# Optimization experiments

Hardware: AMD Instinct MI355X
Metric: run time of the kernel (lower is better)

## Reference

```python
import jax, jax.numpy as jnp
import numpy as np

DIM = 1024
DEPTH = 6
HEADS = 16
MLP = 4096
HEAD_DIM = DIM // HEADS
SCALE = HEAD_DIM ** -0.5
EPS = 1e-5


def _ln(x, g, b):
    m = jnp.mean(x, axis=-1, keepdims=True)
    v = jnp.mean(jnp.square(x - m), axis=-1, keepdims=True)
    return (x - m) * jax.lax.rsqrt(v + EPS) * g + b


def setup_inputs() -> dict:
    key = jax.random.key(0)
    ks = jax.random.split(key, 16)
    B, N = 4, 1024
    s_d = 1.0 / np.sqrt(DIM)
    s_m = 1.0 / np.sqrt(MLP)
    inp = {
        "x1": jax.random.normal(ks[0], (B, N, DIM), jnp.float32),
        "x2": jax.random.normal(ks[1], (B, N, DIM), jnp.float32),
        # stacked per-layer params; Linear weights stored as [in, out]
        "ln1_g": jnp.ones((DEPTH, DIM), jnp.float32),
        "ln1_b": jnp.zeros((DEPTH, DIM), jnp.float32),
        "wq": jax.random.normal(ks[2], (DEPTH, DIM, DIM), jnp.float32) * s_d,
        "wk": jax.random.normal(ks[3], (DEPTH, DIM, DIM), jnp.float32) * s_d,
        "wv": jax.random.normal(ks[4], (DEPTH, DIM, DIM), jnp.float32) * s_d,
        "wo": jax.random.normal(ks[5], (DEPTH, DIM, DIM), jnp.float32) * s_d,
        "bo": jnp.zeros((DEPTH, DIM), jnp.float32),
        "ln2_g": jnp.ones((DEPTH, DIM), jnp.float32),
        "ln2_b": jnp.zeros((DEPTH, DIM), jnp.float32),
        "w1": jax.random.normal(ks[6], (DEPTH, DIM, MLP), jnp.float32) * s_d,
        "b1": jnp.zeros((DEPTH, MLP), jnp.float32),
        "w2": jax.random.normal(ks[7], (DEPTH, MLP, DIM), jnp.float32) * s_m,
        "b2": jnp.zeros((DEPTH, DIM), jnp.float32),
    }
    return inp


def _split_heads(t):
    b, n, _ = t.shape
    return t.reshape(b, n, HEADS, HEAD_DIM).transpose(0, 2, 1, 3)  # b h n d


def reference(x1, x2, ln1_g, ln1_b, wq, wk, wv, wo, bo, ln2_g, ln2_b, w1, b1, w2, b2):
    # dropout disabled (eval mode)
    for i in range(DEPTH):
        # PreNorm(MCA): same LayerNorm params applied to x1 and x2
        n1 = _ln(x1, ln1_g[i], ln1_b[i])
        n2 = _ln(x2, ln1_g[i], ln1_b[i])
        q = _split_heads(n1 @ wq[i])
        k = _split_heads(n2 @ wk[i])
        v = _split_heads(n2 @ wv[i])
        dots = jnp.einsum('bhqd,bhkd->bhqk', q, k) * SCALE
        attn = jax.nn.softmax(dots, axis=-1)
        out = jnp.einsum('bhqk,bhkd->bhqd', attn, v)
        b, h, n, d = out.shape
        out = out.transpose(0, 2, 1, 3).reshape(b, n, h * d)
        x1 = out @ wo[i] + bo[i] + x1
        # PreNorm(FeedForward)
        nf = _ln(x1, ln2_g[i], ln2_b[i])
        hdn = jax.nn.gelu(nf @ w1[i] + b1[i], approximate=False)
        x1 = hdn @ w2[i] + b2[i] + x1
    return x1
```

## Files before the change

### kernel.cpp

```cpp
#include <hip/hip_runtime.h>
#include <stdint.h>

#define N_SEQ 1024
#define N_TOK 4096
#define ATT_SCALE 0.125f

typedef unsigned short u16;
typedef __attribute__((ext_vector_type(8))) short short8;
typedef __attribute__((ext_vector_type(4))) short short4v;
typedef __attribute__((ext_vector_type(4))) float f32x4;

__device__ __forceinline__ u16 f2bf(float f) {
  uint32_t u = __float_as_uint(f);
  u += 0x7fffu + ((u >> 16) & 1u);
  return (u16)(u >> 16);
}

__device__ __forceinline__ void gload16(const void* g, void* lds) {
  __builtin_amdgcn_global_load_lds(
      (const __attribute__((address_space(1))) unsigned int*)g,
      (__attribute__((address_space(3))) unsigned int*)lds, 16, 0, 0);
}

__global__ void copy_f32_kernel(const float* __restrict__ in, float* __restrict__ out) {
  int i = blockIdx.x * 256 + threadIdx.x;
  ((float4*)out)[i] = ((const float4*)in)[i];
}

__global__ __launch_bounds__(256) void tconv_kernel(const float* __restrict__ src,
                                                    u16* __restrict__ dst,
                                                    int K, int NN, size_t dstLS) {
  __shared__ u16 tile[64][68];
  int n0 = blockIdx.x * 64, k0 = blockIdx.y * 64, L = blockIdx.z;
  const float* s = src + (size_t)L * K * NN;
  u16* d = dst + (size_t)L * dstLS;
  int t = threadIdx.x;
  int rr = t >> 4, cc = (t & 15) * 4;
#pragma unroll
  for (int ii = 0; ii < 4; ii++) {
    int kl = rr + ii * 16;
    float4 v = *(const float4*)&s[(size_t)(k0 + kl) * NN + n0 + cc];
    tile[cc + 0][kl] = f2bf(v.x);
    tile[cc + 1][kl] = f2bf(v.y);
    tile[cc + 2][kl] = f2bf(v.z);
    tile[cc + 3][kl] = f2bf(v.w);
  }
  __syncthreads();
#pragma unroll
  for (int ii = 0; ii < 4; ii++) {
    int nl = rr + ii * 16;
    short4v o;
    o.x = (short)tile[nl][cc + 0];
    o.y = (short)tile[nl][cc + 1];
    o.z = (short)tile[nl][cc + 2];
    o.w = (short)tile[nl][cc + 3];
    *(short4v*)&d[(size_t)(n0 + nl) * K + k0 + cc] = o;
  }
}

__global__ __launch_bounds__(256) void ln_kernel(const float* __restrict__ x,
                                                 const float* __restrict__ g,
                                                 const float* __restrict__ b,
                                                 u16* __restrict__ out) {
  int row = blockIdx.x;
  const float* xr = x + (size_t)row * 1024;
  int t = threadIdx.x;
  float4 v = *(const float4*)&xr[t * 4];
  float s = v.x + v.y + v.z + v.w;
  float sq = v.x * v.x + v.y * v.y + v.z * v.z + v.w * v.w;
#pragma unroll
  for (int m = 1; m < 64; m <<= 1) {
    s += __shfl_xor(s, m, 64);
    sq += __shfl_xor(sq, m, 64);
  }
  __shared__ float ps[8];
  int w = t >> 6;
  if ((t & 63) == 0) { ps[w] = s; ps[4 + w] = sq; }
  __syncthreads();
  s = ps[0] + ps[1] + ps[2] + ps[3];
  sq = ps[4] + ps[5] + ps[6] + ps[7];
  float mean = s * (1.0f / 1024.0f);
  float var = sq * (1.0f / 1024.0f) - mean * mean;
  float rs = rsqrtf(var + 1e-5f);
  float4 gv = *(const float4*)&g[t * 4];
  float4 bv = *(const float4*)&b[t * 4];
  short4v o;
  o.x = (short)f2bf((v.x - mean) * rs * gv.x + bv.x);
  o.y = (short)f2bf((v.y - mean) * rs * gv.y + bv.y);
  o.z = (short)f2bf((v.z - mean) * rs * gv.z + bv.z);
  o.w = (short)f2bf((v.w - mean) * rs * gv.w + bv.w);
  *(short4v*)&out[(size_t)row * 1024 + t * 4] = o;
}

template <int MODE>
__global__ __launch_bounds__(256, 3) void gemmM(const u16* __restrict__ A,
                                                const u16* __restrict__ Bt,
                                                u16* __restrict__ outb,
                                                float* __restrict__ outf,
                                                const float* __restrict__ bias,
                                                const float* __restrict__ resid,
                                                int N, int K) {
  constexpr int AT = 128 * 32;
  __shared__ u16 smem[2 * 2 * AT];

  int t = threadIdx.x, lane = t & 63, w = t >> 6;
  int wm = w >> 1, wn = w & 1;
  const u16* Ag = A + (size_t)(blockIdx.y * 128) * K;
  const u16* Bg = Bt + (size_t)(blockIdx.x * 128) * K;
  f32x4 acc[4][4] = {};

  auto stage = [&](int d, int k0) {
    u16* ab = smem + d * 2 * AT;
    u16* bb = ab + AT;
#pragma unroll
    for (int l = 0; l < 2; l++) {
      int c = l * 256 + t;
      gload16(Ag + (size_t)(c >> 2) * K + k0 + (c & 3) * 8, ab + c * 8);
    }
#pragma unroll
    for (int l = 0; l < 2; l++) {
      int c = l * 256 + t;
      gload16(Bg + (size_t)(c >> 2) * K + k0 + (c & 3) * 8, bb + c * 8);
    }
  };

  const int NT = K / 32;
  stage(0, 0);
  __syncthreads();

  int buf = 0;
  for (int tt = 0; tt < NT; tt++) {
    if (tt + 1 < NT) stage(buf ^ 1, (tt + 1) * 32);
    const u16* ab = smem + buf * 2 * AT;
    const u16* bb = ab + AT;
    short8 af[4], bf[4];
#pragma unroll
    for (int mi = 0; mi < 4; mi++)
      af[mi] = *(const short8*)&ab[(wm * 64 + mi * 16 + (lane & 15)) * 32 + (lane >> 4) * 8];
#pragma unroll
    for (int ni = 0; ni < 4; ni++)
      bf[ni] = *(const short8*)&bb[(wn * 64 + ni * 16 + (lane & 15)) * 32 + (lane >> 4) * 8];
#pragma unroll
    for (int mi = 0; mi < 4; mi++)
#pragma unroll
      for (int ni = 0; ni < 4; ni++)
        acc[mi][ni] = __builtin_amdgcn_mfma_f32_16x16x32_bf16(af[mi], bf[ni], acc[mi][ni], 0, 0, 0);
    __syncthreads();
    buf ^= 1;
  }

  int r0 = blockIdx.y * 128 + wm * 64 + ((lane >> 4) << 2);
  int c0 = blockIdx.x * 128 + wn * 64 + (lane & 15);
#pragma unroll
  for (int mi = 0; mi < 4; mi++) {
#pragma unroll
    for (int r = 0; r < 4; r++) {
      size_t row = (size_t)(r0 + mi * 16 + r);
#pragma unroll
      for (int ni = 0; ni < 4; ni++) {
        size_t col = (size_t)(c0 + ni * 16);
        size_t idx = row * N + col;
        float val = acc[mi][ni][r];
        if (MODE == 0) {
          outb[idx] = f2bf(val);
        } else if (MODE == 1) {
          outf[idx] = val + bias[col] + resid[idx];
        } else {
          float xg = val + bias[col];
          outb[idx] = f2bf(0.5f * xg * (1.0f + erff(xg * 0.70710678f)));
        }
      }
    }
  }
}

template <int BM, int BN, int WM, int WN, int MODE>
__global__ __launch_bounds__(WM * WN * 64, 2) void gemm8(const u16* __restrict__ A,
                                                         const u16* __restrict__ Bt,
                                                         u16* __restrict__ outb,
                                                         float* __restrict__ outf,
                                                         const float* __restrict__ bias,
                                                         const float* __restrict__ resid,
                                                         int N, int K) {
  constexpr int BK = 64;
  constexpr int NW = WM * WN;
  constexpr int T = NW * 64;
  constexpr int WTM = BM / WM, WTN = BN / WN;
  constexpr int FM = WTM / 16, FN = WTN / 16, HM = FM / 2;
  constexpr int AT = BM * BK, BTL = BN * BK;
  constexpr int LA = AT / 8 / T, LB = BTL / 8 / T;
  constexpr int LTOT = LA + LB;
  __shared__ u16 smem[2 * (AT + BTL)];

  int t = threadIdx.x, lane = t & 63, w = t >> 6;
  int wm = w / WN, wn = w % WN;
  const u16* Ag = A + (size_t)(blockIdx.y * BM) * K;
  const u16* Bg = Bt + (size_t)(blockIdx.x * BN) * K;
  f32x4 acc[FM][FN] = {};

  auto stage = [&](int d, int k0) {
    u16* ab = smem + d * (AT + BTL);
    u16* bb = ab + AT;
#pragma unroll
    for (int l = 0; l < LA; l++) {
      int c = (l * NW + w) * 64 + lane;
      int r = c >> 3, s = c & 7;
      gload16(Ag + (size_t)r * K + k0 + ((s ^ (r & 7)) << 3), ab + (l * NW + w) * 512);
    }
#pragma unroll
    for (int l = 0; l < LB; l++) {
      int c = (l * NW + w) * 64 + lane;
      int r = c >> 3, s = c & 7;
      gload16(Bg + (size_t)r * K + k0 + ((s ^ (r & 7)) << 3), bb + (l * NW + w) * 512);
    }
  };

  auto rdA = [&](const u16* ab, int mi, int ks) {
    int rr = wm * WTM + mi * 16 + (lane & 15);
    int j = ks * 4 + (lane >> 4);
    return *(const short8*)&ab[rr * BK + ((j ^ (rr & 7)) << 3)];
  };
  auto rdB = [&](const u16* bb, int ni, int ks) {
    int rr = wn * WTN + ni * 16 + (lane & 15);
    int j = ks * 4 + (lane >> 4);
    return *(const short8*)&bb[rr * BK + ((j ^ (rr & 7)) << 3)];
  };

  const int NT = K / BK;
  stage(0, 0);
  stage(1, BK);
  __builtin_amdgcn_sched_barrier(0);

  int buf = 0;
  for (int tt = 0; tt < NT; tt++) {
    asm volatile("s_waitcnt vmcnt(%0)" ::"n"(LTOT) : "memory");
    __builtin_amdgcn_s_barrier();
    __builtin_amdgcn_sched_barrier(0);
    const u16* ab = smem + buf * (AT + BTL);
    const u16* bb = ab + AT;
    short8 b0[FN], a0lo[HM], a0hi[HM], b1[FN], a1lo[HM], a1hi[HM];
#pragma unroll
    for (int n = 0; n < FN; n++) b0[n] = rdB(bb, n, 0);
#pragma unroll
    for (int m = 0; m < HM; m++) a0lo[m] = rdA(ab, m, 0);
#pragma unroll
    for (int m = 0; m < HM; m++) a0hi[m] = rdA(ab, HM + m, 0);
    asm volatile("s_waitcnt lgkmcnt(%0)" ::"n"(HM) : "memory");
    __builtin_amdgcn_sched_barrier(0);
#pragma unroll
    for (int n = 0; n < FN; n++) b1[n] = rdB(bb, n, 1);
#pragma unroll
    for (int m = 0; m < HM; m++) a1lo[m] = rdA(ab, m, 1);
    __builtin_amdgcn_s_setprio(1);
#pragma unroll
    for (int m = 0; m < HM; m++)
#pragma unroll
      for (int n = 0; n < FN; n++)
        acc[m][n] = __builtin_amdgcn_mfma_f32_16x16x32_bf16(a0lo[m], b0[n], acc[m][n], 0, 0, 0);
    __builtin_amdgcn_s_setprio(0);
    asm volatile("s_waitcnt lgkmcnt(%0)" ::"n"(FN + HM) : "memory");
    __builtin_amdgcn_sched_barrier(0);
#pragma unroll
    for (int m = 0; m < HM; m++) a1hi[m] = rdA(ab, HM + m, 1);
    __builtin_amdgcn_s_setprio(1);
#pragma unroll
    for (int m = 0; m < HM; m++)
#pragma unroll
      for (int n = 0; n < FN; n++)
        acc[HM + m][n] = __builtin_amdgcn_mfma_f32_16x16x32_bf16(a0hi[m], b0[n], acc[HM + m][n], 0, 0, 0);
    __builtin_amdgcn_s_setprio(0);
    asm volatile("s_waitcnt lgkmcnt(%0)" ::"n"(HM) : "memory");
    __builtin_amdgcn_sched_barrier(0);
    __builtin_amdgcn_s_setprio(1);
#pragma unroll
    for (int m = 0; m < HM; m++)
#pragma unroll
      for (int n = 0; n < FN; n++)
        acc[m][n] = __builtin_amdgcn_mfma_f32_16x16x32_bf16(a1lo[m], b1[n], acc[m][n], 0, 0, 0);
    __builtin_amdgcn_s_setprio(0);
    asm volatile("s_waitcnt lgkmcnt(0)" ::: "memory");
    __builtin_amdgcn_sched_barrier(0);
    __builtin_amdgcn_s_barrier();
    __builtin_amdgcn_sched_barrier(0);
    stage(buf, ((tt + 2) % NT) * BK);
    __builtin_amdgcn_sched_barrier(0);
    __builtin_amdgcn_s_setprio(1);
#pragma unroll
    for (int m = 0; m < HM; m++)
#pragma unroll
      for (int n = 0; n < FN; n++)
        acc[HM + m][n] = __builtin_amdgcn_mfma_f32_16x16x32_bf16(a1hi[m], b1[n], acc[HM + m][n], 0, 0, 0);
    __builtin_amdgcn_s_setprio(0);
    buf ^= 1;
  }

  int r0 = blockIdx.y * BM + wm * WTM + ((lane >> 4) << 2);
  int c0 = blockIdx.x * BN + wn * WTN + (lane & 15);
#pragma unroll
  for (int mi = 0; mi < FM; mi++) {
#pragma unroll
    for (int r = 0; r < 4; r++) {
      size_t row = (size_t)(r0 + mi * 16 + r);
#pragma unroll
      for (int ni = 0; ni < FN; ni++) {
        size_t col = (size_t)(c0 + ni * 16);
        size_t idx = row * N + col;
        float val = acc[mi][ni][r];
        if (MODE == 0) {
          outb[idx] = f2bf(val);
        } else if (MODE == 1) {
          outf[idx] = val + bias[col] + resid[idx];
        } else {
          float xg = val + bias[col];
          outb[idx] = f2bf(0.5f * xg * (1.0f + erff(xg * 0.70710678f)));
        }
      }
    }
  }
}

__global__ __launch_bounds__(256, 4) void attn_kernel(const u16* __restrict__ qb,
                                                      const u16* __restrict__ kvb,
                                                      u16* __restrict__ ob) {
  int qt = blockIdx.x, bh = blockIdx.y;
  int b = bh >> 4, h = bh & 15;
  int t = threadIdx.x, lane = t & 63, w = t >> 6;
  __shared__ u16 Qs[64 * 64];
  __shared__ u16 Ks[64 * 64];
  __shared__ u16 Vt[64 * 64];
  __shared__ u16 Ps[4][16 * 64];

  const u16* qbase = qb + (size_t)b * N_SEQ * 1024 + h * 64;
  const u16* kbase = kvb + (size_t)b * N_SEQ * 2048 + h * 64;
  const u16* vbase = kbase + 1024;
  u16* obase = ob + (size_t)b * N_SEQ * 1024 + h * 64;

  int r = t >> 2, c = (t & 3) * 16;
  {
    const u16* src = qbase + (size_t)(qt * 64 + r) * 1024 + c;
    *(short8*)&Qs[r * 64 + c] = *(const short8*)src;
    *(short8*)&Qs[r * 64 + c + 8] = *(const short8*)(src + 8);
  }
  short8 kreg0, kreg1, vreg0, vreg1;
  {
    const u16* ksrc = kbase + (size_t)r * 2048 + c;
    kreg0 = *(const short8*)ksrc;
    kreg1 = *(const short8*)(ksrc + 8);
    const u16* vsrc = vbase + (size_t)r * 2048 + c;
    vreg0 = *(const short8*)vsrc;
    vreg1 = *(const short8*)(vsrc + 8);
  }
  __syncthreads();
  short8 qa0 = *(const short8*)&Qs[(w * 16 + (lane & 15)) * 64 + (lane >> 4) * 8];
  short8 qa1 = *(const short8*)&Qs[(w * 16 + (lane & 15)) * 64 + 32 + (lane >> 4) * 8];

  f32x4 o[4] = {};
  float m_r[4] = {-1e30f, -1e30f, -1e30f, -1e30f};
  float l_r[4] = {0.0f, 0.0f, 0.0f, 0.0f};

  for (int kt = 0; kt < 16; kt++) {
    if (kt > 0) __syncthreads();
    {
      int jj0 = c >> 3;
      *(short8*)&Ks[r * 64 + ((jj0 ^ (r & 7)) << 3)] = kreg0;
      *(short8*)&Ks[r * 64 + (((jj0 + 1) ^ (r & 7)) << 3)] = kreg1;
#pragma unroll
      for (int j = 0; j < 8; j++) {
        int row = c + j, rowb = c + 8 + j;
        Vt[row * 64 + (((r >> 3) ^ (row & 7)) << 3) + (r & 7)] = (u16)vreg0[j];
        Vt[rowb * 64 + (((r >> 3) ^ (rowb & 7)) << 3) + (r & 7)] = (u16)vreg1[j];
      }
    }
    __syncthreads();
    if (kt < 15) {
      const u16* ksrc = kbase + (size_t)((kt + 1) * 64 + r) * 2048 + c;
      kreg0 = *(const short8*)ksrc;
      kreg1 = *(const short8*)(ksrc + 8);
      const u16* vsrc = vbase + (size_t)((kt + 1) * 64 + r) * 2048 + c;
      vreg0 = *(const short8*)vsrc;
      vreg1 = *(const short8*)(vsrc + 8);
    }

    f32x4 s[4] = {};
#pragma unroll
    for (int kb = 0; kb < 4; kb++) {
      int key = kb * 16 + (lane & 15);
      int jj = lane >> 4;
      short8 k0 = *(const short8*)&Ks[key * 64 + ((jj ^ (key & 7)) << 3)];
      short8 k1 = *(const short8*)&Ks[key * 64 + (((4 + jj) ^ (key & 7)) << 3)];
      s[kb] = __builtin_amdgcn_mfma_f32_16x16x32_bf16(qa0, k0, s[kb], 0, 0, 0);
      s[kb] = __builtin_amdgcn_mfma_f32_16x16x32_bf16(qa1, k1, s[kb], 0, 0, 0);
    }
    float fac[4], rowsum[4];
#pragma unroll
    for (int rr = 0; rr < 4; rr++) {
      float a = fmaxf(fmaxf(s[0][rr], s[1][rr]), fmaxf(s[2][rr], s[3][rr])) * ATT_SCALE;
      a = fmaxf(a, __shfl_xor(a, 1, 64));
      a = fmaxf(a, __shfl_xor(a, 2, 64));
      a = fmaxf(a, __shfl_xor(a, 4, 64));
      a = fmaxf(a, __shfl_xor(a, 8, 64));
      float mn = fmaxf(m_r[rr], a);
      fac[rr] = __expf(m_r[rr] - mn);
      m_r[rr] = mn;
      rowsum[rr] = 0.0f;
    }
#pragma unroll
    for (int kb = 0; kb < 4; kb++) {
      int chunk = 2 * kb + ((lane & 15) >> 3);
#pragma unroll
      for (int rr = 0; rr < 4; rr++) {
        float p = __expf(s[kb][rr] * ATT_SCALE - m_r[rr]);
        rowsum[rr] += p;
        int row = (lane >> 4) * 4 + rr;
        Ps[w][row * 64 + ((chunk ^ (row & 7)) << 3) + (lane & 7)] = f2bf(p);
      }
    }
#pragma unroll
    for (int rr = 0; rr < 4; rr++) {
      float rs = rowsum[rr];
      rs += __shfl_xor(rs, 1, 64);
      rs += __shfl_xor(rs, 2, 64);
      rs += __shfl_xor(rs, 4, 64);
      rs += __shfl_xor(rs, 8, 64);
      l_r[rr] = l_r[rr] * fac[rr] + rs;
      o[0][rr] *= fac[rr];
      o[1][rr] *= fac[rr];
      o[2][rr] *= fac[rr];
      o[3][rr] *= fac[rr];
    }
#pragma unroll
    for (int ks = 0; ks < 2; ks++) {
      int rowp = lane & 15;
      int jj = 4 * ks + (lane >> 4);
      short8 pf = *(const short8*)&Ps[w][rowp * 64 + ((jj ^ (rowp & 7)) << 3)];
#pragma unroll
      for (int db = 0; db < 4; db++) {
        int row = db * 16 + (lane & 15);
        short8 vf = *(const short8*)&Vt[row * 64 + ((jj ^ (row & 7)) << 3)];
        o[db] = __builtin_amdgcn_mfma_f32_16x16x32_bf16(pf, vf, o[db], 0, 0, 0);
      }
    }
  }
#pragma unroll
  for (int rr = 0; rr < 4; rr++) {
    float inv = 1.0f / l_r[rr];
    size_t row = (size_t)(qt * 64 + w * 16 + (lane >> 4) * 4 + rr);
#pragma unroll
    for (int db = 0; db < 4; db++)
      obase[row * 1024 + db * 16 + (lane & 15)] = f2bf(o[db][rr] * inv);
  }
}

extern "C" void kernel_launch(void* const* d_in, const int* in_sizes, int n_in,
                              void* d_out, int out_size, void* d_ws, size_t ws_size,
                              hipStream_t stream) {
  const float* x1 = (const float*)d_in[0];
  const float* x2 = (const float*)d_in[1];
  const float* ln1_g = (const float*)d_in[2];
  const float* ln1_b = (const float*)d_in[3];
  const float* wq = (const float*)d_in[4];
  const float* wk = (const float*)d_in[5];
  const float* wv = (const float*)d_in[6];
  const float* wo = (const float*)d_in[7];
  const float* bo = (const float*)d_in[8];
  const float* ln2_g = (const float*)d_in[9];
  const float* ln2_b = (const float*)d_in[10];
  const float* w1 = (const float*)d_in[11];
  const float* b1 = (const float*)d_in[12];
  const float* w2 = (const float*)d_in[13];
  const float* b2 = (const float*)d_in[14];
  float* xout = (float*)d_out;

  u16* p = (u16*)d_ws;
  u16* wqt = p;  p += (size_t)6 * 1024 * 1024;
  u16* kvt = p;  p += (size_t)6 * 2048 * 1024;
  u16* wot = p;  p += (size_t)6 * 1024 * 1024;
  u16* w1t = p;  p += (size_t)6 * 4096 * 1024;
  u16* w2t = p;  p += (size_t)6 * 1024 * 4096;
  u16* n1 = p;   p += (size_t)N_TOK * 1024;
  u16* n2 = p;   p += (size_t)N_TOK * 1024;
  u16* qbuf = p; p += (size_t)N_TOK * 1024;
  u16* kvbuf = p; p += (size_t)N_TOK * 2048;
  u16* ao = p;   p += (size_t)N_TOK * 1024;
  u16* hid = p;  p += (size_t)N_TOK * 4096;

  dim3 blk(256);
  tconv_kernel<<<dim3(16, 16, 6), blk, 0, stream>>>(wq, wqt, 1024, 1024, (size_t)1024 * 1024);
  tconv_kernel<<<dim3(16, 16, 6), blk, 0, stream>>>(wk, kvt, 1024, 1024, (size_t)2048 * 1024);
  tconv_kernel<<<dim3(16, 16, 6), blk, 0, stream>>>(wv, kvt + (size_t)1024 * 1024, 1024, 1024, (size_t)2048 * 1024);
  tconv_kernel<<<dim3(16, 16, 6), blk, 0, stream>>>(wo, wot, 1024, 1024, (size_t)1024 * 1024);
  tconv_kernel<<<dim3(64, 16, 6), blk, 0, stream>>>(w1, w1t, 1024, 4096, (size_t)4096 * 1024);
  tconv_kernel<<<dim3(16, 64, 6), blk, 0, stream>>>(w2, w2t, 4096, 1024, (size_t)1024 * 4096);
  copy_f32_kernel<<<4096, blk, 0, stream>>>(x1, xout);

  for (int i = 0; i < 6; i++) {
    ln_kernel<<<N_TOK, blk, 0, stream>>>(xout, ln1_g + i * 1024, ln1_b + i * 1024, n1);
    ln_kernel<<<N_TOK, blk, 0, stream>>>(x2, ln1_g + i * 1024, ln1_b + i * 1024, n2);
    gemm8<128, 64, 2, 2, 0><<<dim3(16, 32), blk, 0, stream>>>(
        n1, wqt + (size_t)i * 1024 * 1024, qbuf, nullptr, nullptr, nullptr, 1024, 1024);
    gemm8<128, 128, 2, 2, 0><<<dim3(16, 32), blk, 0, stream>>>(
        n2, kvt + (size_t)i * 2048 * 1024, kvbuf, nullptr, nullptr, nullptr, 2048, 1024);
    attn_kernel<<<dim3(16, 64), blk, 0, stream>>>(qbuf, kvbuf, ao);
    gemm8<128, 64, 2, 2, 1><<<dim3(16, 32), blk, 0, stream>>>(
        ao, wot + (size_t)i * 1024 * 1024, nullptr, xout, bo + i * 1024, xout, 1024, 1024);
    ln_kernel<<<N_TOK, blk, 0, stream>>>(xout, ln2_g + i * 1024, ln2_b + i * 1024, n1);
    gemmM<2><<<dim3(32, 32), blk, 0, stream>>>(
        n1, w1t + (size_t)i * 4096 * 1024, hid, nullptr, b1 + i * 4096, nullptr, 4096, 1024);
    gemm8<128, 64, 2, 2, 1><<<dim3(16, 32), blk, 0, stream>>>(
        hid, w2t + (size_t)i * 1024 * 4096, nullptr, xout, b2 + i * 1024, xout, 1024, 4096);
  }
}
```

Before: 1.575 ms.

## Hoist K/V projections out of layer loop into one batched GEMM, swizzled BK=64 GEMM

K and V depend only on x2 and per-layer weights, so all six LayerNorms of x2 and all six K/V projections are computed up front. The projections run as one z-batched launch with 6144 blocks, replacing six smaller per-layer launches. A new templated GEMM with BK=64, XOR-swizzled LDS layout and 64x128 tiles replaces the old FFN1 GEMM and is also used for the batched K/V GEMM. This needs workspace for six copies of the normalized x2 and six K/V buffers, and it writes and rereads a larger working set through memory.

```diff
diff --git a/kernel.cpp b/kernel.cpp
--- a/kernel.cpp
+++ b/kernel.cpp
@@ -92,74 +92,99 @@
   *(short4v*)&out[(size_t)row * 1024 + t * 4] = o;
 }
 
-template <int MODE>
-__global__ __launch_bounds__(256, 3) void gemmM(const u16* __restrict__ A,
-                                                const u16* __restrict__ Bt,
-                                                u16* __restrict__ outb,
-                                                float* __restrict__ outf,
-                                                const float* __restrict__ bias,
-                                                const float* __restrict__ resid,
-                                                int N, int K) {
-  constexpr int AT = 128 * 32;
-  __shared__ u16 smem[2 * 2 * AT];
+template <int BM, int BN, int WM, int WN, int MAXB, int MODE>
+__global__ __launch_bounds__(WM * WN * 64, MAXB) void gemmS(const u16* __restrict__ A,
+                                                            const u16* __restrict__ Bt,
+                                                            u16* __restrict__ outb,
+                                                            float* __restrict__ outf,
+                                                            const float* __restrict__ bias,
+                                                            const float* __restrict__ resid,
+                                                            int N, int K,
+                                                            size_t zA, size_t zB, size_t zC) {
+  constexpr int BK = 64;
+  constexpr int NW = WM * WN;
+  constexpr int T = NW * 64;
+  constexpr int WTM = BM / WM, WTN = BN / WN;
+  constexpr int FM = WTM / 16, FN = WTN / 16;
+  constexpr int AT = BM * BK, BTL = BN * BK;
+  constexpr int LA = AT / 8 / T, LB = BTL / 8 / T;
+  __shared__ u16 smem[2 * (AT + BTL)];
 
   int t = threadIdx.x, lane = t & 63, w = t >> 6;
-  int wm = w >> 1, wn = w & 1;
-  const u16* Ag = A + (size_t)(blockIdx.y * 128) * K;
-  const u16* Bg = Bt + (size_t)(blockIdx.x * 128) * K;
-  f32x4 acc[4][4] = {};
+  int wm = w / WN, wn = w % WN;
+  size_t z = blockIdx.z;
+  const u16* Ag = A + z * zA + (size_t)(blockIdx.y * BM) * K;
+  const u16* Bg = Bt + z * zB + (size_t)(blockIdx.x * BN) * K;
+  f32x4 acc[FM][FN] = {};
 
   auto stage = [&](int d, int k0) {
-    u16* ab = smem + d * 2 * AT;
+    u16* ab = smem + d * (AT + BTL);
     u16* bb = ab + AT;
 #pragma unroll
-    for (int l = 0; l < 2; l++) {
-      int c = l * 256 + t;
-      gload16(Ag + (size_t)(c >> 2) * K + k0 + (c & 3) * 8, ab + c * 8);
-    }
-#pragma unroll
-    for (int l = 0; l < 2; l++) {
-      int c = l * 256 + t;
-      gload16(Bg + (size_t)(c >> 2) * K + k0 + (c & 3) * 8, bb + c * 8);
+    for (int l = 0; l < LA; l++) {
+      int c = (l * NW + w) * 64 + lane;
+      int r = c >> 3, s = c & 7;
+      gload16(Ag + (size_t)r * K + k0 + ((s ^ (r & 7)) << 3), ab + (l * NW + w) * 512);
+    }
+#pragma unroll
+    for (int l = 0; l < LB; l++) {
+      int c = (l * NW + w) * 64 + lane;
+      int r = c >> 3, s = c & 7;
+      gload16(Bg + (size_t)r * K + k0 + ((s ^ (r & 7)) << 3), bb + (l * NW + w) * 512);
     }
   };
 
-  const int NT = K / 32;
+  auto rdA = [&](const u16* ab, int mi, int ks) {
+    int rr = wm * WTM + mi * 16 + (lane & 15);
+    int j = ks * 4 + (lane >> 4);
+    return *(const short8*)&ab[rr * BK + ((j ^ (rr & 7)) << 3)];
+  };
+  auto rdB = [&](const u16* bb, int ni, int ks) {
+    int rr = wn * WTN + ni * 16 + (lane & 15);
+    int j = ks * 4 + (lane >> 4);
+    return *(const short8*)&bb[rr * BK + ((j ^ (rr & 7)) << 3)];
+  };
+
+  const int NT = K / BK;
   stage(0, 0);
   __syncthreads();
 
   int buf = 0;
   for (int tt = 0; tt < NT; tt++) {
-    if (tt + 1 < NT) stage(buf ^ 1, (tt + 1) * 32);
-    const u16* ab = smem + buf * 2 * AT;
+    if (tt + 1 < NT) stage(buf ^ 1, (tt + 1) * BK);
+    const u16* ab = smem + buf * (AT + BTL);
     const u16* bb = ab + AT;
-    short8 af[4], bf[4];
-#pragma unroll
-    for (int mi = 0; mi < 4; mi++)
-      af[mi] = *(const short8*)&ab[(wm * 64 + mi * 16 + (lane & 15)) * 32 + (lane >> 4) * 8];
-#pragma unroll
-    for (int ni = 0; ni < 4; ni++)
-      bf[ni] = *(const short8*)&bb[(wn * 64 + ni * 16 + (lane & 15)) * 32 + (lane >> 4) * 8];
-#pragma unroll
-    for (int mi = 0; mi < 4; mi++)
-#pragma unroll
-      for (int ni = 0; ni < 4; ni++)
-        acc[mi][ni] = __builtin_amdgcn_mfma_f32_16x16x32_bf16(af[mi], bf[ni], acc[mi][ni], 0, 0, 0);
+    short8 af[2][FM], bfr[2][FN];
+#pragma unroll
+    for (int ks = 0; ks < 2; ks++) {
+#pragma unroll
+      for (int mi = 0; mi < FM; mi++) af[ks][mi] = rdA(ab, mi, ks);
+#pragma unroll
+      for (int ni = 0; ni < FN; ni++) bfr[ks][ni] = rdB(bb, ni, ks);
+    }
+#pragma unroll
+    for (int ks = 0; ks < 2; ks++)
+#pragma unroll
+      for (int mi = 0; mi < FM; mi++)
+#pragma unroll
+        for (int ni = 0; ni < FN; ni++)
+          acc[mi][ni] = __builtin_amdgcn_mfma_f32_16x16x32_bf16(af[ks][mi], bfr[ks][ni],
+                                                                acc[mi][ni], 0, 0, 0);
     __syncthreads();
     buf ^= 1;
   }
 
-  int r0 = blockIdx.y * 128 + wm * 64 + ((lane >> 4) << 2);
-  int c0 = blockIdx.x * 128 + wn * 64 + (lane & 15);
-#pragma unroll
-  for (int mi = 0; mi < 4; mi++) {
+  int r0 = blockIdx.y * BM + wm * WTM + ((lane >> 4) << 2);
+  int c0 = blockIdx.x * BN + wn * WTN + (lane & 15);
+#pragma unroll
+  for (int mi = 0; mi < FM; mi++) {
 #pragma unroll
     for (int r = 0; r < 4; r++) {
       size_t row = (size_t)(r0 + mi * 16 + r);
 #pragma unroll
-      for (int ni = 0; ni < 4; ni++) {
+      for (int ni = 0; ni < FN; ni++) {
         size_t col = (size_t)(c0 + ni * 16);
-        size_t idx = row * N + col;
+        size_t idx = z * zC + row * N + col;
         float val = acc[mi][ni][r];
         if (MODE == 0) {
           outb[idx] = f2bf(val);
@@ -472,17 +497,17 @@
   float* xout = (float*)d_out;
 
   u16* p = (u16*)d_ws;
-  u16* wqt = p;  p += (size_t)6 * 1024 * 1024;
-  u16* kvt = p;  p += (size_t)6 * 2048 * 1024;
-  u16* wot = p;  p += (size_t)6 * 1024 * 1024;
-  u16* w1t = p;  p += (size_t)6 * 4096 * 1024;
-  u16* w2t = p;  p += (size_t)6 * 1024 * 4096;
-  u16* n1 = p;   p += (size_t)N_TOK * 1024;
-  u16* n2 = p;   p += (size_t)N_TOK * 1024;
-  u16* qbuf = p; p += (size_t)N_TOK * 1024;
-  u16* kvbuf = p; p += (size_t)N_TOK * 2048;
-  u16* ao = p;   p += (size_t)N_TOK * 1024;
-  u16* hid = p;  p += (size_t)N_TOK * 4096;
+  u16* wqt = p;   p += (size_t)6 * 1024 * 1024;
+  u16* kvt = p;   p += (size_t)6 * 2048 * 1024;
+  u16* wot = p;   p += (size_t)6 * 1024 * 1024;
+  u16* w1t = p;   p += (size_t)6 * 4096 * 1024;
+  u16* w2t = p;   p += (size_t)6 * 1024 * 4096;
+  u16* n1 = p;    p += (size_t)N_TOK * 1024;
+  u16* n2all = p; p += (size_t)6 * N_TOK * 1024;
+  u16* qbuf = p;  p += (size_t)N_TOK * 1024;
+  u16* kvb6 = p;  p += (size_t)6 * N_TOK * 2048;
+  u16* ao = p;    p += (size_t)N_TOK * 1024;
+  u16* hid = p;   p += (size_t)N_TOK * 4096;
 
   dim3 blk(256);
   tconv_kernel<<<dim3(16, 16, 6), blk, 0, stream>>>(wq, wqt, 1024, 1024, (size_t)1024 * 1024);
@@ -493,19 +518,23 @@
   tconv_kernel<<<dim3(16, 64, 6), blk, 0, stream>>>(w2, w2t, 4096, 1024, (size_t)1024 * 4096);
   copy_f32_kernel<<<4096, blk, 0, stream>>>(x1, xout);
 
+  for (int i = 0; i < 6; i++)
+    ln_kernel<<<N_TOK, blk, 0, stream>>>(x2, ln1_g + i * 1024, ln1_b + i * 1024,
+                                         n2all + (size_t)i * N_TOK * 1024);
+  gemmS<64, 128, 2, 2, 3, 0><<<dim3(16, 64, 6), blk, 0, stream>>>(
+      n2all, kvt, kvb6, nullptr, nullptr, nullptr, 2048, 1024,
+      (size_t)N_TOK * 1024, (size_t)2048 * 1024, (size_t)N_TOK * 2048);
+
   for (int i = 0; i < 6; i++) {
     ln_kernel<<<N_TOK, blk, 0, stream>>>(xout, ln1_g + i * 1024, ln1_b + i * 1024, n1);
-    ln_kernel<<<N_TOK, blk, 0, stream>>>(x2, ln1_g + i * 1024, ln1_b + i * 1024, n2);
     gemm8<128, 64, 2, 2, 0><<<dim3(16, 32), blk, 0, stream>>>(
         n1, wqt + (size_t)i * 1024 * 1024, qbuf, nullptr, nullptr, nullptr, 1024, 1024);
-    gemm8<128, 128, 2, 2, 0><<<dim3(16, 32), blk, 0, stream>>>(
-        n2, kvt + (size_t)i * 2048 * 1024, kvbuf, nullptr, nullptr, nullptr, 2048, 1024);
-    attn_kernel<<<dim3(16, 64), blk, 0, stream>>>(qbuf, kvbuf, ao);
+    attn_kernel<<<dim3(16, 64), blk, 0, stream>>>(qbuf, kvb6 + (size_t)i * N_TOK * 2048, ao);
     gemm8<128, 64, 2, 2, 1><<<dim3(16, 32), blk, 0, stream>>>(
         ao, wot + (size_t)i * 1024 * 1024, nullptr, xout, bo + i * 1024, xout, 1024, 1024);
     ln_kernel<<<N_TOK, blk, 0, stream>>>(xout, ln2_g + i * 1024, ln2_b + i * 1024, n1);
-    gemmM<2><<<dim3(32, 32), blk, 0, stream>>>(
-        n1, w1t + (size_t)i * 4096 * 1024, hid, nullptr, b1 + i * 4096, nullptr, 4096, 1024);
+    gemmS<64, 128, 2, 2, 3, 2><<<dim3(32, 64), blk, 0, stream>>>(
+        n1, w1t + (size_t)i * 4096 * 1024, hid, nullptr, b1 + i * 4096, nullptr, 4096, 1024, 0, 0, 0);
     gemm8<128, 64, 2, 2, 1><<<dim3(16, 32), blk, 0, stream>>>(
         hid, w2t + (size_t)i * 1024 * 4096, nullptr, xout, b2 + i * 1024, xout, 1024, 4096);
   }
```

Result: no change. 1.585 ms (+0.6%).
